# Optimization experiments

Hardware: AMD Instinct MI355X
Metric: run time of the kernel (lower is better)

The kernel has to match this reference:

```python
import jax, jax.numpy as jnp
import numpy as np

D, P, R, F = 512, 64, 32, 256  # directions, points per ray, rank, virtual subcarriers


def setup_inputs() -> dict:
    key = jax.random.key(0)
    ks = jax.random.split(key, 6)
    return {
        "att_re": jax.random.normal(ks[0], (D, P, R), dtype=jnp.float32),
        "att_im": jax.random.normal(ks[1], (D, P, R), dtype=jnp.float32),
        "rad_re": jax.random.normal(ks[2], (D, P, R), dtype=jnp.float32),
        "rad_im": jax.random.normal(ks[3], (D, P, R), dtype=jnp.float32),
        "freq_re": jax.random.normal(ks[4], (F, R), dtype=jnp.float32),
        "freq_im": jax.random.normal(ks[5], (F, R), dtype=jnp.float32),
        "max_ray_length": 200,
    }


def reference(att_re, att_im, rad_re, rad_im, freq_re, freq_im, max_ray_length):
    att = (att_re + 1j * att_im).astype(jnp.complex64)   # (D,P,R)
    rad = (rad_re + 1j * rad_im).astype(jnp.complex64)   # (D,P,R)
    fv = (freq_re + 1j * freq_im).astype(jnp.complex64)  # (F,R)

    num_points = att.shape[1]
    num_dirs = att.shape[0]
    delta_t = jnp.asarray(max_ray_length / num_points, dtype=jnp.float32)

    # prefix-sum of conjugated attenuation along the ray (u_hat_rho)
    u_hat_rho = jnp.cumsum(att.conj() * delta_t, axis=1)  # (D,P,R)

    # Project each rank-R vector onto each frequency basis vector.
    # The original's v_outer / v_outer_outer einsums factor exactly into these dot products.
    a_proj = jnp.einsum('dpr,fr->dpf', att.conj(), fv)        # (D,P,F)
    r_proj = jnp.einsum('dpr,fr->dpf', rad.conj(), fv)        # (D,P,F)
    u_proj = jnp.einsum('dpr,fr->dpf', u_hat_rho.conj(), fv)  # (D,P,F)

    # first-order: sum over all points; second-order: points k >= 1 only
    first = jnp.sum(r_proj * a_proj, axis=(0, 1))                                   # (F,)
    second = jnp.sum(r_proj[:, 1:] * a_proj[:, 1:] * u_proj[:, 1:], axis=(0, 1))    # (F,)

    csi = (first + second) * delta_t / num_dirs  # (F,) complex64
    return csi
```

## Files before the change

kernel.cpp:

```cpp
#include <hip/hip_runtime.h>

#define ND 512
#define NP 64
#define NR 32
#define NF 256

#define PLANE (ND * NP * NR)
#define BOFF  (6 * PLANE)

typedef __attribute__((ext_vector_type(8))) short bf16x8;
typedef __attribute__((ext_vector_type(4))) float f32x4;

__device__ inline unsigned short f2bf(float x) {
    unsigned u = __builtin_bit_cast(unsigned, x);
    u += 0x7FFFu + ((u >> 16) & 1u);
    return (unsigned short)(u >> 16);
}
__device__ inline unsigned pack2(float a, float b) {
    return (unsigned)f2bf(a) | ((unsigned)f2bf(b) << 16);
}

__global__ __launch_bounds__(256, 2) void lrrt_prep_kernel(
    const float* __restrict__ att_re, const float* __restrict__ att_im,
    const float* __restrict__ rad_re, const float* __restrict__ rad_im,
    const float* __restrict__ freq_re, const float* __restrict__ freq_im,
    unsigned short* __restrict__ ws)
{
    const int t = threadIdx.x;
    const int d = blockIdx.x;
    const size_t base = (size_t)d * (NP * NR);

#pragma unroll
    for (int it = 0; it < 2; ++it) {
        const size_t g = base + (size_t)(t + it * 256) * 4;
        float4 x;
        x = *(const float4*)(att_re + g);
        *(uint2*)(ws + 0 * PLANE + g) = make_uint2(pack2(x.x, x.y), pack2(x.z, x.w));
        x = *(const float4*)(att_im + g);
        *(uint2*)(ws + 1 * PLANE + g) = make_uint2(pack2(x.x, x.y), pack2(x.z, x.w));
        x = *(const float4*)(rad_re + g);
        *(uint2*)(ws + 2 * PLANE + g) = make_uint2(pack2(x.x, x.y), pack2(x.z, x.w));
        x = *(const float4*)(rad_im + g);
        *(uint2*)(ws + 3 * PLANE + g) = make_uint2(pack2(x.x, x.y), pack2(x.z, x.w));
    }

    if (t < 64) {
        const int r = t & 31;
        const int reim = t >> 5;
        const float* src = reim ? att_im : att_re;
        const float sgn = reim ? -1.f : 1.f;
        unsigned short* dst = ws + (size_t)(4 + reim) * PLANE + base;
        float run = src[base + r];
        dst[r] = 0;
#pragma unroll
        for (int p = 1; p < NP; ++p) {
            run += src[base + (size_t)p * NR + r];
            dst[(size_t)p * NR + r] = f2bf(sgn * run);
        }
    }

    if (d < 3) {
        const float* src = (d == 1) ? freq_im : freq_re;
        const float sgn = (d == 2) ? -1.f : 1.f;
        unsigned short* dst = ws + BOFF + (size_t)d * (NF * NR);
        for (int i = t; i < NF * NR; i += 256) dst[i] = f2bf(sgn * src[i]);
    }
}

__global__ __launch_bounds__(256, 4) void lrrt_gemm_kernel(
    const unsigned short* __restrict__ ws, const int* __restrict__ mrl,
    float* __restrict__ out)
{
    __shared__ float s_red[4][NF][2];

    const int t = threadIdx.x;
    const int d = blockIdx.x;
    const int lane = t & 63, wv = t >> 6, kg = lane >> 4, m_lo = lane & 15;

    const size_t arow = (size_t)d * (NP * NR) + (size_t)(wv * 16 + m_lo) * NR + 8 * kg;
    const bf16x8 a_r = *(const bf16x8*)(ws + 0 * PLANE + arow);
    const bf16x8 a_i = *(const bf16x8*)(ws + 1 * PLANE + arow);
    const bf16x8 r_r = *(const bf16x8*)(ws + 2 * PLANE + arow);
    const bf16x8 r_i = *(const bf16x8*)(ws + 3 * PLANE + arow);
    const bf16x8 c_r = *(const bf16x8*)(ws + 4 * PLANE + arow);
    const bf16x8 c_i = *(const bf16x8*)(ws + 5 * PLANE + arow);

    const float dt = (float)(*mrl) / (float)NP;
    const f32x4 zero = {0.f, 0.f, 0.f, 0.f};

#pragma unroll 1
    for (int q = 0; q < 16; ++q) {
        const size_t brow = (size_t)(16 * q + m_lo) * NR + 8 * kg;
        const bf16x8 vr = *(const bf16x8*)(ws + BOFF + brow);
        const bf16x8 vi = *(const bf16x8*)(ws + BOFF + NF * NR + brow);
        const bf16x8 vn = *(const bf16x8*)(ws + BOFF + 2 * NF * NR + brow);

        f32x4 Are = __builtin_amdgcn_mfma_f32_16x16x32_bf16(a_r, vr, zero, 0, 0, 0);
        f32x4 Aim = __builtin_amdgcn_mfma_f32_16x16x32_bf16(a_r, vi, zero, 0, 0, 0);
        f32x4 Bre = __builtin_amdgcn_mfma_f32_16x16x32_bf16(r_r, vr, zero, 0, 0, 0);
        f32x4 Bim = __builtin_amdgcn_mfma_f32_16x16x32_bf16(r_r, vi, zero, 0, 0, 0);
        f32x4 Ure = __builtin_amdgcn_mfma_f32_16x16x32_bf16(c_r, vr, zero, 0, 0, 0);
        f32x4 Uim = __builtin_amdgcn_mfma_f32_16x16x32_bf16(c_r, vi, zero, 0, 0, 0);
        Are = __builtin_amdgcn_mfma_f32_16x16x32_bf16(a_i, vi, Are, 0, 0, 0);
        Aim = __builtin_amdgcn_mfma_f32_16x16x32_bf16(a_i, vn, Aim, 0, 0, 0);
        Bre = __builtin_amdgcn_mfma_f32_16x16x32_bf16(r_i, vi, Bre, 0, 0, 0);
        Bim = __builtin_amdgcn_mfma_f32_16x16x32_bf16(r_i, vn, Bim, 0, 0, 0);
        Ure = __builtin_amdgcn_mfma_f32_16x16x32_bf16(c_i, vi, Ure, 0, 0, 0);
        Uim = __builtin_amdgcn_mfma_f32_16x16x32_bf16(c_i, vn, Uim, 0, 0, 0);

        float sr = 0.f, si = 0.f;
#pragma unroll
        for (int i = 0; i < 4; ++i) {
            const float qre = Bre[i] * Are[i] - Bim[i] * Aim[i];
            const float qim = Bre[i] * Aim[i] + Bim[i] * Are[i];
            const float cre = fmaf(dt, Ure[i], 1.0f);
            const float cim = dt * Uim[i];
            sr = fmaf(qre, cre, fmaf(-qim, cim, sr));
            si = fmaf(qim, cre, fmaf(qre, cim, si));
        }
        sr += __shfl_xor(sr, 16, 64); si += __shfl_xor(si, 16, 64);
        sr += __shfl_xor(sr, 32, 64); si += __shfl_xor(si, 32, 64);
        if (lane < 16) {
            s_red[wv][16 * q + lane][0] = sr;
            s_red[wv][16 * q + lane][1] = si;
        }
    }
    __syncthreads();

    const float scale = dt / (float)ND;
    const int f = t;
    const float re = s_red[0][f][0] + s_red[1][f][0] + s_red[2][f][0] + s_red[3][f][0];
    const float im = s_red[0][f][1] + s_red[1][f][1] + s_red[2][f][1] + s_red[3][f][1];
    atomicAdd(&out[f], re * scale);
    atomicAdd(&out[NF + f], im * scale);
}

extern "C" void kernel_launch(void* const* d_in, const int* in_sizes, int n_in,
                              void* d_out, int out_size, void* d_ws, size_t ws_size,
                              hipStream_t stream) {
    const float* att_re = (const float*)d_in[0];
    const float* att_im = (const float*)d_in[1];
    const float* rad_re = (const float*)d_in[2];
    const float* rad_im = (const float*)d_in[3];
    const float* freq_re = (const float*)d_in[4];
    const float* freq_im = (const float*)d_in[5];
    const int* mrl = (const int*)d_in[6];
    float* out = (float*)d_out;
    unsigned short* ws = (unsigned short*)d_ws;

    hipMemsetAsync(d_out, 0, (size_t)out_size * sizeof(float), stream);

    lrrt_prep_kernel<<<ND, 256, 0, stream>>>(
        att_re, att_im, rad_re, rad_im, freq_re, freq_im, ws);
    lrrt_gemm_kernel<<<ND, 256, 0, stream>>>(ws, mrl, out);
}
```

Measured before the change: 108.1 us.

## Fuse bf16 conversion and prefix-sum into main kernel via LDS staging

Drops the global bf16 workspace for the attenuation, radiance and cumsum planes. Each block now converts its direction's data into padded shared memory and computes the prefix sum in parallel across four segments before running the MFMA loop. The grid is split into two halves over frequency, so each direction is loaded and converted twice. The frequency-only prep becomes a tiny kernel, the negated imaginary plane is produced by a sign-bit flip, and dt is folded into the cumsum values. This removes the large global write and readback of the intermediate planes, at the cost of redundant per-block conversion and extra LDS use.

```diff
diff --git a/kernel.cpp b/kernel.cpp
--- a/kernel.cpp
+++ b/kernel.cpp
@@ -4,12 +4,11 @@
 #define NP 64
 #define NR 32
 #define NF 256
-
-#define PLANE (ND * NP * NR)
-#define BOFF  (6 * PLANE)
+#define RS 40
 
 typedef __attribute__((ext_vector_type(8))) short bf16x8;
 typedef __attribute__((ext_vector_type(4))) float f32x4;
+typedef __attribute__((ext_vector_type(4))) unsigned int uint4v;
 
 __device__ inline unsigned short f2bf(float x) {
     unsigned u = __builtin_bit_cast(unsigned, x);
@@ -19,81 +18,106 @@
 __device__ inline unsigned pack2(float a, float b) {
     return (unsigned)f2bf(a) | ((unsigned)f2bf(b) << 16);
 }
+__device__ inline bf16x8 neg8(bf16x8 v) {
+    uint4v u = __builtin_bit_cast(uint4v, v);
+    u ^= (uint4v){0x80008000u, 0x80008000u, 0x80008000u, 0x80008000u};
+    return __builtin_bit_cast(bf16x8, u);
+}
 
-__global__ __launch_bounds__(256, 2) void lrrt_prep_kernel(
+__global__ __launch_bounds__(256) void lrrt_bprep_kernel(
+    const float* __restrict__ fre, const float* __restrict__ fim,
+    unsigned short* __restrict__ ws)
+{
+    const int tid = blockIdx.x * 256 + threadIdx.x;
+    const int plane = tid >> 11;
+    const int i4 = (tid & 2047) * 4;
+    const float* src = plane ? fim : fre;
+    const float4 x = *(const float4*)(src + i4);
+    *(uint2*)(ws + plane * (NF * NR) + i4) = make_uint2(pack2(x.x, x.y), pack2(x.z, x.w));
+}
+
+__global__ __launch_bounds__(256, 4) void lrrt_main_kernel(
     const float* __restrict__ att_re, const float* __restrict__ att_im,
     const float* __restrict__ rad_re, const float* __restrict__ rad_im,
-    const float* __restrict__ freq_re, const float* __restrict__ freq_im,
-    unsigned short* __restrict__ ws)
+    const unsigned short* __restrict__ wsB, const int* __restrict__ mrl,
+    float* __restrict__ out)
 {
+    __shared__ __align__(16) unsigned short s_a[6][NP * RS];
+    __shared__ float s_tot[256];
+    __shared__ float s_red[4][128][2];
+
     const int t = threadIdx.x;
-    const int d = blockIdx.x;
+    const int h = blockIdx.x & 1;
+    const int d = blockIdx.x >> 1;
     const size_t base = (size_t)d * (NP * NR);
+    const int lane = t & 63, wv = t >> 6, kg = lane >> 4, m_lo = lane & 15;
+    const float dt = (float)(*mrl) / (float)NP;
 
 #pragma unroll
-    for (int it = 0; it < 2; ++it) {
-        const size_t g = base + (size_t)(t + it * 256) * 4;
+    for (int half = 0; half < 2; ++half) {
+        const int w = t + half * 256;
+        const int p = w >> 3;
+        const int c = (w & 7) * 4;
+        const size_t g = base + (size_t)p * NR + c;
+        const int lo = p * RS + c;
         float4 x;
         x = *(const float4*)(att_re + g);
-        *(uint2*)(ws + 0 * PLANE + g) = make_uint2(pack2(x.x, x.y), pack2(x.z, x.w));
+        *(uint2*)&s_a[0][lo] = make_uint2(pack2(x.x, x.y), pack2(x.z, x.w));
         x = *(const float4*)(att_im + g);
-        *(uint2*)(ws + 1 * PLANE + g) = make_uint2(pack2(x.x, x.y), pack2(x.z, x.w));
+        *(uint2*)&s_a[1][lo] = make_uint2(pack2(x.x, x.y), pack2(x.z, x.w));
         x = *(const float4*)(rad_re + g);
-        *(uint2*)(ws + 2 * PLANE + g) = make_uint2(pack2(x.x, x.y), pack2(x.z, x.w));
+        *(uint2*)&s_a[2][lo] = make_uint2(pack2(x.x, x.y), pack2(x.z, x.w));
         x = *(const float4*)(rad_im + g);
-        *(uint2*)(ws + 3 * PLANE + g) = make_uint2(pack2(x.x, x.y), pack2(x.z, x.w));
+        *(uint2*)&s_a[3][lo] = make_uint2(pack2(x.x, x.y), pack2(x.z, x.w));
     }
 
-    if (t < 64) {
-        const int r = t & 31;
-        const int reim = t >> 5;
-        const float* src = reim ? att_im : att_re;
-        const float sgn = reim ? -1.f : 1.f;
-        unsigned short* dst = ws + (size_t)(4 + reim) * PLANE + base;
-        float run = src[base + r];
-        dst[r] = 0;
+    const int cs_r = t & 31, cs_reim = (t >> 5) & 1, cs_seg = t >> 6;
+    float vals[16];
+    {
+        const float* src = cs_reim ? att_im : att_re;
+        float run = 0.f;
 #pragma unroll
-        for (int p = 1; p < NP; ++p) {
-            run += src[base + (size_t)p * NR + r];
-            dst[(size_t)p * NR + r] = f2bf(sgn * run);
+        for (int i = 0; i < 16; ++i) {
+            run += src[base + (size_t)(cs_seg * 16 + i) * NR + cs_r];
+            vals[i] = run;
+        }
+        s_tot[t] = run;
+    }
+    __syncthreads();
+
+    {
+        float off = 0.f;
+#pragma unroll
+        for (int s = 0; s < 3; ++s)
+            if (s < cs_seg) off += s_tot[s * 64 + cs_reim * 32 + cs_r];
+        const float sc = cs_reim ? -dt : dt;
+        unsigned short* dst = s_a[4 + cs_reim];
+#pragma unroll
+        for (int i = 0; i < 16; ++i) {
+            const int p = cs_seg * 16 + i;
+            dst[p * RS + cs_r] = (p == 0) ? (unsigned short)0
+                                          : f2bf(sc * (vals[i] + off));
         }
     }
+    __syncthreads();
 
-    if (d < 3) {
-        const float* src = (d == 1) ? freq_im : freq_re;
-        const float sgn = (d == 2) ? -1.f : 1.f;
-        unsigned short* dst = ws + BOFF + (size_t)d * (NF * NR);
-        for (int i = t; i < NF * NR; i += 256) dst[i] = f2bf(sgn * src[i]);
-    }
-}
+    const int aoff = (wv * 16 + m_lo) * RS + 8 * kg;
+    const bf16x8 a_r = *(const bf16x8*)&s_a[0][aoff];
+    const bf16x8 a_i = *(const bf16x8*)&s_a[1][aoff];
+    const bf16x8 r_r = *(const bf16x8*)&s_a[2][aoff];
+    const bf16x8 r_i = *(const bf16x8*)&s_a[3][aoff];
+    const bf16x8 c_r = *(const bf16x8*)&s_a[4][aoff];
+    const bf16x8 c_i = *(const bf16x8*)&s_a[5][aoff];
 
-__global__ __launch_bounds__(256, 4) void lrrt_gemm_kernel(
-    const unsigned short* __restrict__ ws, const int* __restrict__ mrl,
-    float* __restrict__ out)
-{
-    __shared__ float s_red[4][NF][2];
-
-    const int t = threadIdx.x;
-    const int d = blockIdx.x;
-    const int lane = t & 63, wv = t >> 6, kg = lane >> 4, m_lo = lane & 15;
-
-    const size_t arow = (size_t)d * (NP * NR) + (size_t)(wv * 16 + m_lo) * NR + 8 * kg;
-    const bf16x8 a_r = *(const bf16x8*)(ws + 0 * PLANE + arow);
-    const bf16x8 a_i = *(const bf16x8*)(ws + 1 * PLANE + arow);
-    const bf16x8 r_r = *(const bf16x8*)(ws + 2 * PLANE + arow);
-    const bf16x8 r_i = *(const bf16x8*)(ws + 3 * PLANE + arow);
-    const bf16x8 c_r = *(const bf16x8*)(ws + 4 * PLANE + arow);
-    const bf16x8 c_i = *(const bf16x8*)(ws + 5 * PLANE + arow);
-
-    const float dt = (float)(*mrl) / (float)NP;
     const f32x4 zero = {0.f, 0.f, 0.f, 0.f};
 
 #pragma unroll 1
-    for (int q = 0; q < 16; ++q) {
-        const size_t brow = (size_t)(16 * q + m_lo) * NR + 8 * kg;
-        const bf16x8 vr = *(const bf16x8*)(ws + BOFF + brow);
-        const bf16x8 vi = *(const bf16x8*)(ws + BOFF + NF * NR + brow);
-        const bf16x8 vn = *(const bf16x8*)(ws + BOFF + 2 * NF * NR + brow);
+    for (int q = 0; q < 8; ++q) {
+        const int f = 16 * (8 * h + q) + m_lo;
+        const size_t boff = (size_t)f * NR + 8 * kg;
+        const bf16x8 vr = *(const bf16x8*)(wsB + boff);
+        const bf16x8 vi = *(const bf16x8*)(wsB + NF * NR + boff);
+        const bf16x8 vn = neg8(vr);
 
         f32x4 Are = __builtin_amdgcn_mfma_f32_16x16x32_bf16(a_r, vr, zero, 0, 0, 0);
         f32x4 Aim = __builtin_amdgcn_mfma_f32_16x16x32_bf16(a_r, vi, zero, 0, 0, 0);
@@ -113,8 +137,8 @@
         for (int i = 0; i < 4; ++i) {
             const float qre = Bre[i] * Are[i] - Bim[i] * Aim[i];
             const float qim = Bre[i] * Aim[i] + Bim[i] * Are[i];
-            const float cre = fmaf(dt, Ure[i], 1.0f);
-            const float cim = dt * Uim[i];
+            const float cre = 1.0f + Ure[i];
+            const float cim = Uim[i];
             sr = fmaf(qre, cre, fmaf(-qim, cim, sr));
             si = fmaf(qim, cre, fmaf(qre, cim, si));
         }
@@ -128,11 +152,12 @@
     __syncthreads();
 
     const float scale = dt / (float)ND;
-    const int f = t;
-    const float re = s_red[0][f][0] + s_red[1][f][0] + s_red[2][f][0] + s_red[3][f][0];
-    const float im = s_red[0][f][1] + s_red[1][f][1] + s_red[2][f][1] + s_red[3][f][1];
-    atomicAdd(&out[f], re * scale);
-    atomicAdd(&out[NF + f], im * scale);
+    {
+        const int lf = t >> 1, comp = t & 1;
+        const float v = s_red[0][lf][comp] + s_red[1][lf][comp]
+                      + s_red[2][lf][comp] + s_red[3][lf][comp];
+        atomicAdd(&out[comp * NF + h * 128 + lf], v * scale);
+    }
 }
 
 extern "C" void kernel_launch(void* const* d_in, const int* in_sizes, int n_in,
@@ -150,7 +175,7 @@
 
     hipMemsetAsync(d_out, 0, (size_t)out_size * sizeof(float), stream);
 
-    lrrt_prep_kernel<<<ND, 256, 0, stream>>>(
-        att_re, att_im, rad_re, rad_im, freq_re, freq_im, ws);
-    lrrt_gemm_kernel<<<ND, 256, 0, stream>>>(ws, mrl, out);
+    lrrt_bprep_kernel<<<16, 256, 0, stream>>>(freq_re, freq_im, ws);
+    lrrt_main_kernel<<<2 * ND, 256, 0, stream>>>(
+        att_re, att_im, rad_re, rad_im, ws, mrl, out);
 }
```

Result: faster. 96.74 us (-10.5%).
